# Performance work log

Hardware: AMD Instinct MI355X
Metric: run time of the kernel (lower is better)

Reference implementation:

```python
import jax, jax.numpy as jnp
import numpy as np

NB_HEAD = 16
DIM_PER_HEAD = 64
EMB = 1024
B, SQ, SK = 4, 2048, 2048


def setup_inputs() -> dict:
    key = jax.random.key(0)
    ks = jax.random.split(key, 8)
    scale = 1.0 / np.sqrt(EMB)
    return {
        "hidden_state_query": jax.random.normal(ks[0], (B, SQ, EMB), jnp.float32),
        "hidden_state_key": jax.random.normal(ks[1], (B, SK, EMB), jnp.float32),
        "hidden_state_value": jax.random.normal(ks[2], (B, SK, EMB), jnp.float32),
        "attention_mask": jax.random.randint(ks[3], (B, SQ, SK), 0, 2).astype(bool),
        "Wq": jax.random.uniform(ks[4], (NB_HEAD * DIM_PER_HEAD, EMB), jnp.float32, -scale, scale),
        "Wk": jax.random.uniform(ks[5], (NB_HEAD * DIM_PER_HEAD, EMB), jnp.float32, -scale, scale),
        "Wv": jax.random.uniform(ks[6], (NB_HEAD * DIM_PER_HEAD, EMB), jnp.float32, -scale, scale),
        "Wo": jax.random.uniform(ks[7], (EMB, NB_HEAD * DIM_PER_HEAD), jnp.float32, -scale, scale),
    }


def reference(hidden_state_query, hidden_state_key, hidden_state_value,
              attention_mask, Wq, Wk, Wv, Wo):
    bs, sq, _ = hidden_state_query.shape
    sk = hidden_state_key.shape[1]
    # projections (nn.Linear without bias: x @ W.T)
    q = (hidden_state_query @ Wq.T).reshape(bs, sq, NB_HEAD, DIM_PER_HEAD).transpose(0, 2, 1, 3)
    k = (hidden_state_key @ Wk.T).reshape(bs, sk, NB_HEAD, DIM_PER_HEAD).transpose(0, 2, 1, 3)
    v = (hidden_state_value @ Wv.T).reshape(bs, sk, NB_HEAD, DIM_PER_HEAD).transpose(0, 2, 1, 3)
    scores = jnp.einsum('bhqd,bhkd->bhqk', q, k) / jnp.sqrt(jnp.asarray(DIM_PER_HEAD, q.dtype))
    attn = jax.nn.softmax(scores, axis=-1)
    # POST-softmax zero masking (True -> 0), broadcast over heads; no renormalization
    attn = jnp.where(attention_mask[:, None, :, :], jnp.asarray(0.0, attn.dtype), attn)
    ctx = jnp.einsum('bhqk,bhkd->bhqd', attn, v)  # [B,H,Sq,Dh]
    ctx = ctx.transpose(0, 2, 1, 3).reshape(bs, sq, NB_HEAD * DIM_PER_HEAD)
    return ctx @ Wo.T + hidden_state_query
```

## Files before the change

kernel.cpp:

```cpp
#include <hip/hip_runtime.h>
#include <hip/hip_bf16.h>
#include <stdint.h>

typedef __bf16 bf16_t;
typedef bf16_t bf16x8 __attribute__((ext_vector_type(8)));
typedef float  f32x4  __attribute__((ext_vector_type(4)));
typedef float  f32x16 __attribute__((ext_vector_type(16)));
typedef unsigned uint2v __attribute__((ext_vector_type(2)));

#define NB_HEAD 16
#define DH      64
#define EMB     1024
#define BATCH   4
#define SEQ     2048
#define NTOK    (BATCH*SEQ)

#define QSCALE 0.1803368801111204f

__device__ __forceinline__ void gload_lds16(const void* g, void* l) {
  __builtin_amdgcn_global_load_lds(
      (const __attribute__((address_space(1))) void*)g,
      (__attribute__((address_space(3))) void*)l, 16, 0, 0);
}

__device__ __forceinline__ uint32_t pkbf(float a, float b) {
  uint16_t ua = __builtin_bit_cast(uint16_t, (bf16_t)a);
  uint16_t ub = __builtin_bit_cast(uint16_t, (bf16_t)b);
  return (uint32_t)ua | ((uint32_t)ub << 16);
}

__global__ void cvt_f32_bf16(const float* __restrict__ in,
                             bf16_t* __restrict__ out, int n8) {
  int i = blockIdx.x * blockDim.x + threadIdx.x;
  if (i >= n8) return;
  const float4* p = reinterpret_cast<const float4*>(in) + (size_t)i * 2;
  float4 a = p[0], b = p[1];
  bf16x8 v;
  v[0] = (bf16_t)a.x; v[1] = (bf16_t)a.y; v[2] = (bf16_t)a.z; v[3] = (bf16_t)a.w;
  v[4] = (bf16_t)b.x; v[5] = (bf16_t)b.y; v[6] = (bf16_t)b.z; v[7] = (bf16_t)b.w;
  reinterpret_cast<bf16x8*>(out)[i] = v;
}

__global__ void mkand(const uint8_t* __restrict__ m, uint16_t* __restrict__ out,
                      int n8) {
  int i = blockIdx.x * blockDim.x + threadIdx.x;
  if (i >= n8) return;
  uint2 v = reinterpret_cast<const uint2*>(m)[i];
  uint4 r;
  uint32_t lo = v.x, hi = v.y;
  uint16_t e[8];
#pragma unroll
  for (int j = 0; j < 4; j++) e[j]     = (uint16_t)(((lo >> (8 * j)) & 0xFF) - 1);
#pragma unroll
  for (int j = 0; j < 4; j++) e[4 + j] = (uint16_t)(((hi >> (8 * j)) & 0xFF) - 1);
  r.x = (uint32_t)e[0] | ((uint32_t)e[1] << 16);
  r.y = (uint32_t)e[2] | ((uint32_t)e[3] << 16);
  r.z = (uint32_t)e[4] | ((uint32_t)e[5] << 16);
  r.w = (uint32_t)e[6] | ((uint32_t)e[7] << 16);
  reinterpret_cast<uint4*>(out)[i] = r;
}

#define BM 128
#define BN 128
#define BKT 64

template<int EPI>
__global__ void __launch_bounds__(256, 2)
gemm_bt(const bf16_t* __restrict__ A, const bf16_t* __restrict__ Bw,
        bf16_t* __restrict__ Cb, float* __restrict__ Cf,
        const float* __restrict__ resid, float qscale) {
  __shared__ bf16_t As[2][BM * BKT];
  __shared__ bf16_t Bs[2][BN * BKT];
  const int K = EMB, N = EMB;
  const int t    = threadIdx.x;
  const int lane = t & 63, w = t >> 6;
  const int wr = w >> 1, wc = w & 1;
  const int l15 = lane & 15, l4 = lane >> 4;

  const int lin = blockIdx.x + 8 * blockIdx.y;
  const int nl  = (lin & 7) * 64 + (lin >> 3);
  const int rowBase = (nl >> 3) * BM, colBase = (nl & 7) * BN;

  f32x4 acc[4][4];
#pragma unroll
  for (int i = 0; i < 4; i++)
#pragma unroll
    for (int j = 0; j < 4; j++) acc[i][j] = f32x4{0.f, 0.f, 0.f, 0.f};

  const int lin16 = w * 1024 + lane * 16;

#pragma unroll
  for (int i = 0; i < 4; ++i) {
    int off  = i * 4096 + lin16;
    int row  = off >> 7, colb = off & 127;
    gload_lds16((const char*)A  + (((size_t)(rowBase + row)) * K) * 2 + colb, (char*)As[0] + off);
    gload_lds16((const char*)Bw + (((size_t)(colBase + row)) * K) * 2 + colb, (char*)Bs[0] + off);
  }
  __syncthreads();

  int cur = 0;
  for (int k0 = 0; k0 < K; k0 += BKT) {
    if (k0 + BKT < K) {
      const int nb = cur ^ 1;
#pragma unroll
      for (int i = 0; i < 4; ++i) {
        int off  = i * 4096 + lin16;
        int row  = off >> 7, colb = off & 127;
        gload_lds16((const char*)A  + (((size_t)(rowBase + row)) * K + k0 + BKT) * 2 + colb, (char*)As[nb] + off);
        gload_lds16((const char*)Bw + (((size_t)(colBase + row)) * K + k0 + BKT) * 2 + colb, (char*)Bs[nb] + off);
      }
    }
#pragma unroll
    for (int kc = 0; kc < 2; ++kc) {
      bf16x8 af[4], bfb[4];
#pragma unroll
      for (int mi = 0; mi < 4; mi++)
        af[mi] = *reinterpret_cast<const bf16x8*>(
            &As[cur][(wr * 64 + mi * 16 + l15) * BKT + kc * 32 + l4 * 8]);
#pragma unroll
      for (int ni = 0; ni < 4; ni++)
        bfb[ni] = *reinterpret_cast<const bf16x8*>(
            &Bs[cur][(wc * 64 + ni * 16 + l15) * BKT + kc * 32 + l4 * 8]);
      __builtin_amdgcn_s_setprio(1);
#pragma unroll
      for (int mi = 0; mi < 4; mi++)
#pragma unroll
        for (int ni = 0; ni < 4; ni++)
          acc[mi][ni] = __builtin_amdgcn_mfma_f32_16x16x32_bf16(
              af[mi], bfb[ni], acc[mi][ni], 0, 0, 0);
      __builtin_amdgcn_s_setprio(0);
    }
    __syncthreads();
    cur ^= 1;
  }

#pragma unroll
  for (int mi = 0; mi < 4; mi++) {
#pragma unroll
    for (int ni = 0; ni < 4; ni++) {
      const int m0 = rowBase + wr * 64 + mi * 16 + l4 * 4;
      const int n  = colBase + wc * 64 + ni * 16 + l15;
      if (EPI == 1) {
        size_t base = ((size_t)((m0 >> 11) * 1024 + n)) * 2048 + (m0 & 2047);
        uint2 st;
        st.x = pkbf(acc[mi][ni][0], acc[mi][ni][1]);
        st.y = pkbf(acc[mi][ni][2], acc[mi][ni][3]);
        *reinterpret_cast<uint2*>(Cb + base) = st;
      } else {
#pragma unroll
        for (int r = 0; r < 4; r++) {
          int m = m0 + r;
          float v = acc[mi][ni][r];
          if (EPI == 0) {
            Cb[(size_t)m * N + n] = (bf16_t)(v * qscale);
          } else if (EPI == 3) {
            Cb[(((size_t)((m >> 11) * 16 + (n >> 6))) * 2048 + (m & 2047)) * 64 + (n & 63)] = (bf16_t)v;
          } else {
            Cf[(size_t)m * N + n] = v + resid[(size_t)m * N + n];
          }
        }
      }
    }
  }
}

__global__ void __launch_bounds__(512, 2)
attn32(const bf16_t* __restrict__ Qb, const bf16_t* __restrict__ Kh,
       const bf16_t* __restrict__ Vt, const uint16_t* __restrict__ Mand,
       bf16_t* __restrict__ ctx) {
  __shared__ __align__(16) bf16_t Ks[2][64 * 64];
  __shared__ __align__(16) bf16_t Vs[2][64 * 64];

  const int t = threadIdx.x, lane = t & 63, wid = t >> 6;
  const int q = lane & 31, hi = lane >> 5;

  const int lin = blockIdx.x + 8 * (blockIdx.y + 16 * blockIdx.z);
  const int nl  = (lin & 7) * 64 + (lin >> 3);
  const int bx = nl & 7, h = (nl >> 3) & 15, b = nl >> 7;

  const int q0 = bx * 256 + wid * 32;
  const int qrow = b * SEQ + q0 + q;

  const int srow  = t >> 3;
  const int scolx = ((t & 7) ^ ((t >> 3) & 7)) * 16;
  const char* kg = (const char*)(Kh + ((size_t)(b * NB_HEAD + h)) * SEQ * DH);
  const char* vg = (const char*)(Vt + ((size_t)(b * NB_HEAD + h)) * DH * SEQ);

  const bf16_t* qp = Qb + (size_t)qrow * EMB + h * DH + hi * 8;
  bf16x8 qf[4];
#pragma unroll
  for (int d = 0; d < 4; d++) qf[d] = *reinterpret_cast<const bf16x8*>(qp + d * 16);

  f32x16 o0 = {0}, o1 = {0};
  float lrun = 0.f;
  const uint16_t* mbase = Mand + (size_t)qrow * SEQ;
  const int qx = (q & 7) << 4;

  gload_lds16(kg + (size_t)srow * 128 + scolx,  (char*)Ks[0] + t * 16);
  gload_lds16(vg + (size_t)srow * 4096 + scolx, (char*)Vs[0] + t * 16);
  __syncthreads();

  int cur = 0;
  for (int kb = 0; kb < SEQ; kb += 64) {
    if (kb + 64 < SEQ) {
      const int nb = cur ^ 1;
      gload_lds16(kg + (size_t)(kb + 64) * 128 + (size_t)srow * 128 + scolx,
                  (char*)Ks[nb] + t * 16);
      gload_lds16(vg + (size_t)(kb + 64) * 2 + (size_t)srow * 4096 + scolx,
                  (char*)Vs[nb] + t * 16);
    }

    const char* kls = (const char*)Ks[cur];
    f32x16 p0 = {0}, p1 = {0};
    __builtin_amdgcn_s_setprio(1);
#pragma unroll
    for (int dsl = 0; dsl < 4; dsl++) {
      const int cb = (dsl * 32 + hi * 16) ^ qx;
      bf16x8 kf0 = *reinterpret_cast<const bf16x8*>(kls + q * 128 + cb);
      bf16x8 kf1 = *reinterpret_cast<const bf16x8*>(kls + (32 + q) * 128 + cb);
      p0 = __builtin_amdgcn_mfma_f32_32x32x16_bf16(kf0, qf[dsl], p0, 0, 0, 0);
      p1 = __builtin_amdgcn_mfma_f32_32x32x16_bf16(kf1, qf[dsl], p1, 0, 0, 0);
    }
    __builtin_amdgcn_s_setprio(0);

    uint4 mv[4];
#pragma unroll
    for (int ks = 0; ks < 4; ks++)
      mv[ks] = *reinterpret_cast<const uint4*>(mbase + kb + 16 * ks + 8 * hi);

    float ps = 0.f;
#pragma unroll
    for (int i = 0; i < 16; i++) { p0[i] = __builtin_amdgcn_exp2f(p0[i]); ps += p0[i]; }
#pragma unroll
    for (int i = 0; i < 16; i++) { p1[i] = __builtin_amdgcn_exp2f(p1[i]); ps += p1[i]; }
    ps += __shfl_xor(ps, 32);
    lrun += ps;

    const char* vls = (const char*)Vs[cur];
#pragma unroll
    for (int ks = 0; ks < 4; ks++) {
      const int s8 = (ks & 1) * 8;
      float e0, e1, e2, e3, e4, e5, e6, e7;
      if (ks < 2) {
        e0 = p0[s8+0]; e1 = p0[s8+1]; e2 = p0[s8+2]; e3 = p0[s8+3];
        e4 = p0[s8+4]; e5 = p0[s8+5]; e6 = p0[s8+6]; e7 = p0[s8+7];
      } else {
        e0 = p1[s8+0]; e1 = p1[s8+1]; e2 = p1[s8+2]; e3 = p1[s8+3];
        e4 = p1[s8+4]; e5 = p1[s8+5]; e6 = p1[s8+6]; e7 = p1[s8+7];
      }
      uint32_t a0 = pkbf(e0, e1), a1 = pkbf(e2, e3);
      uint32_t a2 = pkbf(e4, e5), a3 = pkbf(e6, e7);
      uint2v s02 = __builtin_amdgcn_permlane32_swap(a0, a2, false, false);
      uint2v s13 = __builtin_amdgcn_permlane32_swap(a1, a3, false, false);
      uint4 fr;
      fr.x = s02[0]; fr.y = s13[0]; fr.z = s02[1]; fr.w = s13[1];
      fr.x &= mv[ks].x; fr.y &= mv[ks].y; fr.z &= mv[ks].z; fr.w &= mv[ks].w;
      bf16x8 pa = __builtin_bit_cast(bf16x8, fr);
      const int cb = (ks * 32 + hi * 16) ^ qx;
      bf16x8 vf0 = *reinterpret_cast<const bf16x8*>(vls + q * 128 + cb);
      bf16x8 vf1 = *reinterpret_cast<const bf16x8*>(vls + (32 + q) * 128 + cb);
      __builtin_amdgcn_s_setprio(1);
      o0 = __builtin_amdgcn_mfma_f32_32x32x16_bf16(vf0, pa, o0, 0, 0, 0);
      o1 = __builtin_amdgcn_mfma_f32_32x32x16_bf16(vf1, pa, o1, 0, 0, 0);
      __builtin_amdgcn_s_setprio(0);
    }

    __syncthreads();
    cur ^= 1;
  }

  float inv = 1.0f / lrun;
  bf16_t* cp = ctx + (size_t)qrow * EMB + h * DH;
#pragma unroll
  for (int g = 0; g < 4; g++) {
    uint2 st;
    st.x = pkbf(o0[4*g+0] * inv, o0[4*g+1] * inv);
    st.y = pkbf(o0[4*g+2] * inv, o0[4*g+3] * inv);
    *reinterpret_cast<uint2*>(cp + 8 * g + 4 * hi) = st;
    st.x = pkbf(o1[4*g+0] * inv, o1[4*g+1] * inv);
    st.y = pkbf(o1[4*g+2] * inv, o1[4*g+3] * inv);
    *reinterpret_cast<uint2*>(cp + 32 + 8 * g + 4 * hi) = st;
  }
}

extern "C" void kernel_launch(void* const* d_in, const int* in_sizes, int n_in,
                              void* d_out, int out_size, void* d_ws, size_t ws_size,
                              hipStream_t stream) {
  const float*   hq   = (const float*)d_in[0];
  const float*   hk   = (const float*)d_in[1];
  const float*   hv   = (const float*)d_in[2];
  const uint8_t* mask = (const uint8_t*)d_in[3];
  const float*   Wq   = (const float*)d_in[4];
  const float*   Wk   = (const float*)d_in[5];
  const float*   Wv   = (const float*)d_in[6];
  const float*   Wo   = (const float*)d_in[7];
  float* out = (float*)d_out;

  char* ws = (char*)d_ws;
  const size_t SZ_H = (size_t)NTOK * EMB * 2;
  const size_t SZ_W = (size_t)EMB * EMB * 2;
  bf16_t* hq_b = (bf16_t*)(ws + 0 * SZ_H);
  bf16_t* hk_b = (bf16_t*)(ws + 1 * SZ_H);
  bf16_t* hv_b = (bf16_t*)(ws + 2 * SZ_H);
  bf16_t* Qb   = (bf16_t*)(ws + 3 * SZ_H);
  bf16_t* Kh   = (bf16_t*)(ws + 4 * SZ_H);
  bf16_t* Vt   = (bf16_t*)(ws + 5 * SZ_H);
  bf16_t* ctx  = (bf16_t*)(ws + 6 * SZ_H);
  bf16_t* Wq_b = (bf16_t*)(ws + 7 * SZ_H + 0 * SZ_W);
  bf16_t* Wk_b = (bf16_t*)(ws + 7 * SZ_H + 1 * SZ_W);
  bf16_t* Wv_b = (bf16_t*)(ws + 7 * SZ_H + 2 * SZ_W);
  bf16_t* Wo_b = (bf16_t*)(ws + 7 * SZ_H + 3 * SZ_W);
  uint16_t* Mand = (uint16_t*)(ws + 0);

  const int n8h = NTOK * EMB / 8;
  const int n8w = EMB * EMB / 8;
  cvt_f32_bf16<<<n8h / 256, 256, 0, stream>>>(hq, hq_b, n8h);
  cvt_f32_bf16<<<n8h / 256, 256, 0, stream>>>(hk, hk_b, n8h);
  cvt_f32_bf16<<<n8h / 256, 256, 0, stream>>>(hv, hv_b, n8h);
  cvt_f32_bf16<<<n8w / 256, 256, 0, stream>>>(Wq, Wq_b, n8w);
  cvt_f32_bf16<<<n8w / 256, 256, 0, stream>>>(Wk, Wk_b, n8w);
  cvt_f32_bf16<<<n8w / 256, 256, 0, stream>>>(Wv, Wv_b, n8w);
  cvt_f32_bf16<<<n8w / 256, 256, 0, stream>>>(Wo, Wo_b, n8w);

  dim3 ggrid(EMB / BN, NTOK / BM);
  gemm_bt<0><<<ggrid, 256, 0, stream>>>(hq_b, Wq_b, Qb, nullptr, nullptr, QSCALE);
  gemm_bt<3><<<ggrid, 256, 0, stream>>>(hk_b, Wk_b, Kh, nullptr, nullptr, 1.0f);
  gemm_bt<1><<<ggrid, 256, 0, stream>>>(hv_b, Wv_b, Vt, nullptr, nullptr, 1.0f);

  const int n8m = BATCH * SEQ * SEQ / 8;
  mkand<<<n8m / 256, 256, 0, stream>>>(mask, Mand, n8m);

  attn32<<<dim3(SEQ / 256, NB_HEAD, BATCH), 512, 0, stream>>>(Qb, Kh, Vt, Mand, ctx);

  gemm_bt<2><<<ggrid, 256, 0, stream>>>(ctx, Wo_b, nullptr, out, hq, 1.0f);
}
```

Measured before the change: 258.7 us.

## Fuse prep kernels, widen attention KV tile, compute row sums via MFMA

Result: no change. 255.3 us (-1.3%).

```diff
diff --git a/kernel.cpp b/kernel.cpp
--- a/kernel.cpp
+++ b/kernel.cpp
@@ -3,6 +3,7 @@
 #include <stdint.h>
 
 typedef __bf16 bf16_t;
+typedef bf16_t bf16x2 __attribute__((ext_vector_type(2)));
 typedef bf16_t bf16x8 __attribute__((ext_vector_type(8)));
 typedef float  f32x4  __attribute__((ext_vector_type(4)));
 typedef float  f32x16 __attribute__((ext_vector_type(16)));
@@ -24,27 +25,22 @@
 }
 
 __device__ __forceinline__ uint32_t pkbf(float a, float b) {
-  uint16_t ua = __builtin_bit_cast(uint16_t, (bf16_t)a);
-  uint16_t ub = __builtin_bit_cast(uint16_t, (bf16_t)b);
-  return (uint32_t)ua | ((uint32_t)ub << 16);
-}
-
-__global__ void cvt_f32_bf16(const float* __restrict__ in,
-                             bf16_t* __restrict__ out, int n8) {
-  int i = blockIdx.x * blockDim.x + threadIdx.x;
-  if (i >= n8) return;
+  bf16x2 v = { (bf16_t)a, (bf16_t)b };
+  return __builtin_bit_cast(uint32_t, v);
+}
+
+__device__ __forceinline__ void cvt8_body(const float* __restrict__ in,
+                                          bf16_t* __restrict__ out, int i) {
   const float4* p = reinterpret_cast<const float4*>(in) + (size_t)i * 2;
   float4 a = p[0], b = p[1];
-  bf16x8 v;
-  v[0] = (bf16_t)a.x; v[1] = (bf16_t)a.y; v[2] = (bf16_t)a.z; v[3] = (bf16_t)a.w;
-  v[4] = (bf16_t)b.x; v[5] = (bf16_t)b.y; v[6] = (bf16_t)b.z; v[7] = (bf16_t)b.w;
-  reinterpret_cast<bf16x8*>(out)[i] = v;
-}
-
-__global__ void mkand(const uint8_t* __restrict__ m, uint16_t* __restrict__ out,
-                      int n8) {
-  int i = blockIdx.x * blockDim.x + threadIdx.x;
-  if (i >= n8) return;
+  uint4 r;
+  r.x = pkbf(a.x, a.y); r.y = pkbf(a.z, a.w);
+  r.z = pkbf(b.x, b.y); r.w = pkbf(b.z, b.w);
+  reinterpret_cast<uint4*>(out)[i] = r;
+}
+
+__device__ __forceinline__ void mkand_body(const uint8_t* __restrict__ m,
+                                           uint16_t* __restrict__ out, int i) {
   uint2 v = reinterpret_cast<const uint2*>(m)[i];
   uint4 r;
   uint32_t lo = v.x, hi = v.y;
@@ -58,6 +54,36 @@
   r.z = (uint32_t)e[4] | ((uint32_t)e[5] << 16);
   r.w = (uint32_t)e[6] | ((uint32_t)e[7] << 16);
   reinterpret_cast<uint4*>(out)[i] = r;
+}
+
+__global__ void __launch_bounds__(256)
+prep(const float* __restrict__ hq, const float* __restrict__ hk,
+     const float* __restrict__ hv, const float* __restrict__ Wq,
+     const float* __restrict__ Wk, const float* __restrict__ Wv,
+     const float* __restrict__ Wo,
+     bf16_t* hq_b, bf16_t* hk_b, bf16_t* hv_b,
+     bf16_t* Wq_b, bf16_t* Wk_b, bf16_t* Wv_b, bf16_t* Wo_b,
+     const uint8_t* __restrict__ mask, uint16_t* __restrict__ mand) {
+  const int bid = blockIdx.x;
+  if (bid < 12288) {
+    const int seg = bid >> 12;
+    const float* src = seg == 0 ? hq : seg == 1 ? hk : hv;
+    bf16_t*      dst = seg == 0 ? hq_b : seg == 1 ? hk_b : hv_b;
+    cvt8_body(src, dst, (bid & 4095) * 256 + (int)threadIdx.x);
+  } else if (bid < 14336) {
+    const int sb = bid - 12288;
+    const int seg = sb >> 9;
+    const float* src = seg == 0 ? Wq : seg == 1 ? Wk : seg == 2 ? Wv : Wo;
+    bf16_t*      dst = seg == 0 ? Wq_b : seg == 1 ? Wk_b : seg == 2 ? Wv_b : Wo_b;
+    cvt8_body(src, dst, (sb & 511) * 256 + (int)threadIdx.x);
+  } else {
+    mkand_body(mask, mand, (bid - 14336) * 256 + (int)threadIdx.x);
+  }
+}
+
+__global__ void __launch_bounds__(256)
+mkand(const uint8_t* __restrict__ m, uint16_t* __restrict__ out) {
+  mkand_body(m, out, blockIdx.x * 256 + (int)threadIdx.x);
 }
 
 #define BM 128
@@ -164,12 +190,14 @@
   }
 }
 
-__global__ void __launch_bounds__(512, 2)
+#define KVB 128
+
+__global__ void __launch_bounds__(512, 4)
 attn32(const bf16_t* __restrict__ Qb, const bf16_t* __restrict__ Kh,
        const bf16_t* __restrict__ Vt, const uint16_t* __restrict__ Mand,
        bf16_t* __restrict__ ctx) {
-  __shared__ __align__(16) bf16_t Ks[2][64 * 64];
-  __shared__ __align__(16) bf16_t Vs[2][64 * 64];
+  __shared__ __align__(16) bf16_t Ks[2][KVB * 64];
+  __shared__ __align__(16) bf16_t Vs[2][64 * KVB];
 
   const int t = threadIdx.x, lane = t & 63, wid = t >> 6;
   const int q = lane & 31, hi = lane >> 5;
@@ -181,8 +209,10 @@
   const int q0 = bx * 256 + wid * 32;
   const int qrow = b * SEQ + q0 + q;
 
-  const int srow  = t >> 3;
-  const int scolx = ((t & 7) ^ ((t >> 3) & 7)) * 16;
+  const int srow8  = t >> 3;
+  const int scol8  = ((t & 7) ^ ((t >> 3) & 7)) * 16;
+  const int srow16 = t >> 4;
+  const int scol16 = (((t & 15) ^ ((t >> 4) & 7)) & 15) * 16;
   const char* kg = (const char*)(Kh + ((size_t)(b * NB_HEAD + h)) * SEQ * DH);
   const char* vg = (const char*)(Vt + ((size_t)(b * NB_HEAD + h)) * DH * SEQ);
 
@@ -191,85 +221,95 @@
 #pragma unroll
   for (int d = 0; d < 4; d++) qf[d] = *reinterpret_cast<const bf16x8*>(qp + d * 16);
 
-  f32x16 o0 = {0}, o1 = {0};
-  float lrun = 0.f;
+  bf16x8 ones;
+#pragma unroll
+  for (int i = 0; i < 8; i++) ones[i] = (bf16_t)1.0f;
+
+  f32x16 o0 = {0}, o1 = {0}, sacc = {0};
   const uint16_t* mbase = Mand + (size_t)qrow * SEQ;
   const int qx = (q & 7) << 4;
 
-  gload_lds16(kg + (size_t)srow * 128 + scolx,  (char*)Ks[0] + t * 16);
-  gload_lds16(vg + (size_t)srow * 4096 + scolx, (char*)Vs[0] + t * 16);
+  gload_lds16(kg + (size_t)srow8 * 128 + scol8,                 (char*)Ks[0] + t * 16);
+  gload_lds16(kg + (size_t)(64 + srow8) * 128 + scol8,          (char*)Ks[0] + 8192 + t * 16);
+  gload_lds16(vg + (size_t)srow16 * 4096 + scol16,              (char*)Vs[0] + t * 16);
+  gload_lds16(vg + (size_t)(32 + srow16) * 4096 + scol16,       (char*)Vs[0] + 8192 + t * 16);
   __syncthreads();
 
   int cur = 0;
-  for (int kb = 0; kb < SEQ; kb += 64) {
-    if (kb + 64 < SEQ) {
+#pragma unroll 1
+  for (int kb = 0; kb < SEQ; kb += KVB) {
+    if (kb + KVB < SEQ) {
       const int nb = cur ^ 1;
-      gload_lds16(kg + (size_t)(kb + 64) * 128 + (size_t)srow * 128 + scolx,
-                  (char*)Ks[nb] + t * 16);
-      gload_lds16(vg + (size_t)(kb + 64) * 2 + (size_t)srow * 4096 + scolx,
-                  (char*)Vs[nb] + t * 16);
-    }
-
-    const char* kls = (const char*)Ks[cur];
-    f32x16 p0 = {0}, p1 = {0};
-    __builtin_amdgcn_s_setprio(1);
-#pragma unroll
-    for (int dsl = 0; dsl < 4; dsl++) {
-      const int cb = (dsl * 32 + hi * 16) ^ qx;
-      bf16x8 kf0 = *reinterpret_cast<const bf16x8*>(kls + q * 128 + cb);
-      bf16x8 kf1 = *reinterpret_cast<const bf16x8*>(kls + (32 + q) * 128 + cb);
-      p0 = __builtin_amdgcn_mfma_f32_32x32x16_bf16(kf0, qf[dsl], p0, 0, 0, 0);
-      p1 = __builtin_amdgcn_mfma_f32_32x32x16_bf16(kf1, qf[dsl], p1, 0, 0, 0);
-    }
-    __builtin_amdgcn_s_setprio(0);
-
-    uint4 mv[4];
-#pragma unroll
-    for (int ks = 0; ks < 4; ks++)
-      mv[ks] = *reinterpret_cast<const uint4*>(mbase + kb + 16 * ks + 8 * hi);
-
-    float ps = 0.f;
-#pragma unroll
-    for (int i = 0; i < 16; i++) { p0[i] = __builtin_amdgcn_exp2f(p0[i]); ps += p0[i]; }
-#pragma unroll
-    for (int i = 0; i < 16; i++) { p1[i] = __builtin_amdgcn_exp2f(p1[i]); ps += p1[i]; }
-    ps += __shfl_xor(ps, 32);
-    lrun += ps;
-
-    const char* vls = (const char*)Vs[cur];
-#pragma unroll
-    for (int ks = 0; ks < 4; ks++) {
-      const int s8 = (ks & 1) * 8;
-      float e0, e1, e2, e3, e4, e5, e6, e7;
-      if (ks < 2) {
-        e0 = p0[s8+0]; e1 = p0[s8+1]; e2 = p0[s8+2]; e3 = p0[s8+3];
-        e4 = p0[s8+4]; e5 = p0[s8+5]; e6 = p0[s8+6]; e7 = p0[s8+7];
-      } else {
-        e0 = p1[s8+0]; e1 = p1[s8+1]; e2 = p1[s8+2]; e3 = p1[s8+3];
-        e4 = p1[s8+4]; e5 = p1[s8+5]; e6 = p1[s8+6]; e7 = p1[s8+7];
+      const size_t kO = (size_t)(kb + KVB) * 128;
+      const size_t vO = (size_t)(kb + KVB) * 2;
+      gload_lds16(kg + kO + (size_t)srow8 * 128 + scol8,           (char*)Ks[nb] + t * 16);
+      gload_lds16(kg + kO + (size_t)(64 + srow8) * 128 + scol8,    (char*)Ks[nb] + 8192 + t * 16);
+      gload_lds16(vg + vO + (size_t)srow16 * 4096 + scol16,        (char*)Vs[nb] + t * 16);
+      gload_lds16(vg + vO + (size_t)(32 + srow16) * 4096 + scol16, (char*)Vs[nb] + 8192 + t * 16);
+    }
+
+#pragma unroll
+    for (int hh = 0; hh < 2; hh++) {
+      const char* kls = (const char*)Ks[cur] + hh * 8192;
+      f32x16 p0 = {0}, p1 = {0};
+      __builtin_amdgcn_s_setprio(1);
+#pragma unroll
+      for (int dsl = 0; dsl < 4; dsl++) {
+        const int cb = (dsl * 32 + hi * 16) ^ qx;
+        bf16x8 kf0 = *reinterpret_cast<const bf16x8*>(kls + q * 128 + cb);
+        bf16x8 kf1 = *reinterpret_cast<const bf16x8*>(kls + (32 + q) * 128 + cb);
+        p0 = __builtin_amdgcn_mfma_f32_32x32x16_bf16(kf0, qf[dsl], p0, 0, 0, 0);
+        p1 = __builtin_amdgcn_mfma_f32_32x32x16_bf16(kf1, qf[dsl], p1, 0, 0, 0);
       }
-      uint32_t a0 = pkbf(e0, e1), a1 = pkbf(e2, e3);
-      uint32_t a2 = pkbf(e4, e5), a3 = pkbf(e6, e7);
-      uint2v s02 = __builtin_amdgcn_permlane32_swap(a0, a2, false, false);
-      uint2v s13 = __builtin_amdgcn_permlane32_swap(a1, a3, false, false);
-      uint4 fr;
-      fr.x = s02[0]; fr.y = s13[0]; fr.z = s02[1]; fr.w = s13[1];
-      fr.x &= mv[ks].x; fr.y &= mv[ks].y; fr.z &= mv[ks].z; fr.w &= mv[ks].w;
-      bf16x8 pa = __builtin_bit_cast(bf16x8, fr);
-      const int cb = (ks * 32 + hi * 16) ^ qx;
-      bf16x8 vf0 = *reinterpret_cast<const bf16x8*>(vls + q * 128 + cb);
-      bf16x8 vf1 = *reinterpret_cast<const bf16x8*>(vls + (32 + q) * 128 + cb);
-      __builtin_amdgcn_s_setprio(1);
-      o0 = __builtin_amdgcn_mfma_f32_32x32x16_bf16(vf0, pa, o0, 0, 0, 0);
-      o1 = __builtin_amdgcn_mfma_f32_32x32x16_bf16(vf1, pa, o1, 0, 0, 0);
       __builtin_amdgcn_s_setprio(0);
+
+      uint4 mv[4];
+#pragma unroll
+      for (int ks = 0; ks < 4; ks++)
+        mv[ks] = *reinterpret_cast<const uint4*>(mbase + kb + 64 * hh + 16 * ks + 8 * hi);
+
+      const char* vls = (const char*)Vs[cur];
+
+#pragma unroll
+      for (int i = 0; i < 16; i++) p0[i] = __builtin_amdgcn_exp2f(p0[i]);
+
+#pragma unroll
+      for (int half = 0; half < 2; half++) {
+        if (half == 1) {
+#pragma unroll
+          for (int i = 0; i < 16; i++) p1[i] = __builtin_amdgcn_exp2f(p1[i]);
+        }
+        const f32x16& ph = half ? p1 : p0;
+#pragma unroll
+        for (int kss = 0; kss < 2; kss++) {
+          const int ks = half * 2 + kss;
+          const int s8 = kss * 8;
+          uint32_t a0 = pkbf(ph[s8+0], ph[s8+1]), a1 = pkbf(ph[s8+2], ph[s8+3]);
+          uint32_t a2 = pkbf(ph[s8+4], ph[s8+5]), a3 = pkbf(ph[s8+6], ph[s8+7]);
+          uint2v s02 = __builtin_amdgcn_permlane32_swap(a0, a2, false, false);
+          uint2v s13 = __builtin_amdgcn_permlane32_swap(a1, a3, false, false);
+          uint4 fr;
+          fr.x = s02[0]; fr.y = s13[0]; fr.z = s02[1]; fr.w = s13[1];
+          bf16x8 pa_raw = __builtin_bit_cast(bf16x8, fr);
+          sacc = __builtin_amdgcn_mfma_f32_32x32x16_bf16(ones, pa_raw, sacc, 0, 0, 0);
+          fr.x &= mv[ks].x; fr.y &= mv[ks].y; fr.z &= mv[ks].z; fr.w &= mv[ks].w;
+          bf16x8 pa = __builtin_bit_cast(bf16x8, fr);
+          const int cbv = (hh * 128 + ks * 32 + hi * 16) ^ qx;
+          bf16x8 vf0 = *reinterpret_cast<const bf16x8*>(vls + q * 256 + cbv);
+          bf16x8 vf1 = *reinterpret_cast<const bf16x8*>(vls + (32 + q) * 256 + cbv);
+          __builtin_amdgcn_s_setprio(1);
+          o0 = __builtin_amdgcn_mfma_f32_32x32x16_bf16(vf0, pa, o0, 0, 0, 0);
+          o1 = __builtin_amdgcn_mfma_f32_32x32x16_bf16(vf1, pa, o1, 0, 0, 0);
+          __builtin_amdgcn_s_setprio(0);
+        }
+      }
     }
 
     __syncthreads();
     cur ^= 1;
   }
 
-  float inv = 1.0f / lrun;
+  float inv = 1.0f / sacc[0];
   bf16_t* cp = ctx + (size_t)qrow * EMB + h * DH;
 #pragma unroll
   for (int g = 0; g < 4; g++) {
@@ -310,25 +350,22 @@
   bf16_t* Wk_b = (bf16_t*)(ws + 7 * SZ_H + 1 * SZ_W);
   bf16_t* Wv_b = (bf16_t*)(ws + 7 * SZ_H + 2 * SZ_W);
   bf16_t* Wo_b = (bf16_t*)(ws + 7 * SZ_H + 3 * SZ_W);
-  uint16_t* Mand = (uint16_t*)(ws + 0);
-
-  const int n8h = NTOK * EMB / 8;
-  const int n8w = EMB * EMB / 8;
-  cvt_f32_bf16<<<n8h / 256, 256, 0, stream>>>(hq, hq_b, n8h);
-  cvt_f32_bf16<<<n8h / 256, 256, 0, stream>>>(hk, hk_b, n8h);
-  cvt_f32_bf16<<<n8h / 256, 256, 0, stream>>>(hv, hv_b, n8h);
-  cvt_f32_bf16<<<n8w / 256, 256, 0, stream>>>(Wq, Wq_b, n8w);
-  cvt_f32_bf16<<<n8w / 256, 256, 0, stream>>>(Wk, Wk_b, n8w);
-  cvt_f32_bf16<<<n8w / 256, 256, 0, stream>>>(Wv, Wv_b, n8w);
-  cvt_f32_bf16<<<n8w / 256, 256, 0, stream>>>(Wo, Wo_b, n8w);
+
+  const size_t MAND_OFF = 7 * SZ_H + 4 * SZ_W;
+  const size_t MAND_SZ  = (size_t)BATCH * SEQ * SEQ * 2;
+  const bool bigws = ws_size >= MAND_OFF + MAND_SZ;
+  uint16_t* Mand = bigws ? (uint16_t*)(ws + MAND_OFF) : (uint16_t*)ws;
+
+  prep<<<bigws ? 22528 : 14336, 256, 0, stream>>>(
+      hq, hk, hv, Wq, Wk, Wv, Wo,
+      hq_b, hk_b, hv_b, Wq_b, Wk_b, Wv_b, Wo_b, mask, Mand);
 
   dim3 ggrid(EMB / BN, NTOK / BM);
   gemm_bt<0><<<ggrid, 256, 0, stream>>>(hq_b, Wq_b, Qb, nullptr, nullptr, QSCALE);
   gemm_bt<3><<<ggrid, 256, 0, stream>>>(hk_b, Wk_b, Kh, nullptr, nullptr, 1.0f);
   gemm_bt<1><<<ggrid, 256, 0, stream>>>(hv_b, Wv_b, Vt, nullptr, nullptr, 1.0f);
 
-  const int n8m = BATCH * SEQ * SEQ / 8;
-  mkand<<<n8m / 256, 256, 0, stream>>>(mask, Mand, n8m);
+  if (!bigws) mkand<<<8192, 256, 0, stream>>>(mask, Mand);
 
   attn32<<<dim3(SEQ / 256, NB_HEAD, BATCH), 512, 0, stream>>>(Qb, Kh, Vt, Mand, ctx);
 
```
